# Kernel tuning notes

Hardware: AMD Instinct MI355X
Metric: run time of the kernel (lower is better)

## Reference

```python
import jax, jax.numpy as jnp
import numpy as np

N, M, E, DIM = 100000, 2000, 400000, 128
GIN = 2 * DIM + 3  # gate MLP input width


def _mlp2(x, W1, b1, W2, b2):
    # Linear -> ReLU -> Linear
    return jnp.maximum(x @ W1 + b1, 0.0) @ W2 + b2


def setup_inputs() -> dict:
    key = jax.random.key(0)
    ks = jax.random.split(key, 20)
    s = lambda fan_in: 1.0 / np.sqrt(fan_in)
    inp = {
        "res_feat": jax.random.normal(ks[0], (N, DIM), jnp.float32),
        "meta_feat": jax.random.normal(ks[1], (M, DIM), jnp.float32),
        "sec_ids": jax.random.randint(ks[2], (N,), 0, M),
        "batch_pe_vector": jax.random.normal(ks[3], (N, 3), jnp.float32),
        "batch_meta_2_node_edge": jax.random.randint(ks[4], (2, E), 0, M),
        "batch_meta_2_node_vector": jax.random.normal(ks[5], (E, 3), jnp.float32),
        # gate1 params
        "g1_W1": jax.random.uniform(ks[6], (GIN, DIM), jnp.float32, -s(GIN), s(GIN)),
        "g1_b1": jnp.zeros((DIM,), jnp.float32),
        "g1_W2": jax.random.uniform(ks[7], (DIM, DIM), jnp.float32, -s(DIM), s(DIM)),
        "g1_b2": jnp.zeros((DIM,), jnp.float32),
        # gate2 params
        "g2_W1": jax.random.uniform(ks[8], (GIN, DIM), jnp.float32, -s(GIN), s(GIN)),
        "g2_b1": jnp.zeros((DIM,), jnp.float32),
        "g2_W2": jax.random.uniform(ks[9], (DIM, DIM), jnp.float32, -s(DIM), s(DIM)),
        "g2_b2": jnp.zeros((DIM,), jnp.float32),
        # fuse params
        "f_W1": jax.random.uniform(ks[10], (DIM, DIM), jnp.float32, -s(DIM), s(DIM)),
        "f_b1": jnp.zeros((DIM,), jnp.float32),
        "f_W2": jax.random.uniform(ks[11], (DIM, DIM), jnp.float32, -s(DIM), s(DIM)),
        "f_b2": jnp.zeros((DIM,), jnp.float32),
    }
    return inp


def reference(res_feat, meta_feat, sec_ids, batch_pe_vector,
              batch_meta_2_node_edge, batch_meta_2_node_vector,
              g1_W1, g1_b1, g1_W2, g1_b2,
              g2_W1, g2_b1, g2_W2, g2_b2,
              f_W1, f_b1, f_W2, f_b2):
    n = res_feat.shape[0]
    # gate1: per-node gather of meta features
    meta_broadcast = meta_feat[sec_ids]                       # [N, dim]
    gate1_in = jnp.concatenate([res_feat, meta_broadcast, -batch_pe_vector], axis=-1)
    gate1_w = _mlp2(gate1_in, g1_W1, g1_b1, g1_W2, g1_b2)     # [N, dim]
    # gate2: per-edge gathers
    src, dst = batch_meta_2_node_edge[0], batch_meta_2_node_edge[1]
    meta_add = meta_feat[src]                                 # [E, dim]
    res_b = res_feat[dst]                                     # [E, dim]
    gate2_in = jnp.concatenate([res_b, meta_add, batch_meta_2_node_vector], axis=-1)
    gate2_w = _mlp2(gate2_in, g2_W1, g2_b1, g2_W2, g2_b2)     # [E, dim]
    # scatter_mean over destination nodes
    vals = gate2_w * meta_add
    sums = jax.ops.segment_sum(vals, dst, num_segments=n)
    cnts = jax.ops.segment_sum(jnp.ones((vals.shape[0],), vals.dtype), dst, num_segments=n)
    meta_add_fea = sums / jnp.maximum(cnts, 1.0)[:, None]
    fused = res_feat + gate1_w * meta_broadcast + meta_add_fea
    return _mlp2(fused, f_W1, f_b1, f_W2, f_b2)
```

## Files before the change

kernel.cpp:

```cpp
#include <hip/hip_runtime.h>


typedef short bf16x8 __attribute__((ext_vector_type(8)));
typedef float f32x4  __attribute__((ext_vector_type(4)));

#define XS_PAD 136

__device__ __forceinline__ unsigned short f2bf(float f){
  union { float f; unsigned u; } v; v.f = f;
  return (unsigned short)((v.u + 0x7FFFu + ((v.u >> 16) & 1u)) >> 16);
}
__device__ __forceinline__ unsigned pack2(float a, float b){
  return (unsigned)f2bf(a) | ((unsigned)f2bf(b) << 16);
}

__device__ __forceinline__ void mfma_layer(const unsigned short* Xs,
                                           const bf16x8 (&B)[2][4],
                                           int lane, f32x4 (&acc)[4][2]) {
  const int lcol = lane & 15, quad = lane >> 4;
  #pragma unroll
  for (int rg = 0; rg < 4; ++rg) {
    bf16x8 A[4];
    const unsigned short* ab = Xs + (rg*16 + lcol)*XS_PAD + quad*8;
    #pragma unroll
    for (int kk = 0; kk < 4; ++kk) A[kk] = *(const bf16x8*)(ab + kk*32);
    #pragma unroll
    for (int ctl = 0; ctl < 2; ++ctl)
      #pragma unroll
      for (int kk = 0; kk < 4; ++kk)
        acc[rg][ctl] = __builtin_amdgcn_mfma_f32_16x16x32_bf16(
            A[kk], B[ctl][kk], acc[rg][ctl], 0, 0, 0);
  }
}

__device__ __forceinline__ void load_bfrags(const unsigned short* __restrict__ Wt,
                                            int wave, int lane, bf16x8 (&B)[2][4]) {
  const int lcol = lane & 15, quad = lane >> 4;
  #pragma unroll
  for (int ctl = 0; ctl < 2; ++ctl) {
    int col = (wave*2 + ctl)*16 + lcol;
    #pragma unroll
    for (int kk = 0; kk < 4; ++kk)
      B[ctl][kk] = *(const bf16x8*)(Wt + (size_t)col*128 + kk*32 + quad*8);
  }
}

__device__ __forceinline__ void zero_acc(f32x4 (&acc)[4][2]) {
  #pragma unroll
  for (int rg = 0; rg < 4; ++rg)
    #pragma unroll
    for (int ctl = 0; ctl < 2; ++ctl) {
      acc[rg][ctl][0]=0.f; acc[rg][ctl][1]=0.f;
      acc[rg][ctl][2]=0.f; acc[rg][ctl][3]=0.f;
    }
}

struct WPtrs { const float* s[8]; };
__global__ __launch_bounds__(256) void transpose_w8(WPtrs p,
                                                    unsigned short* __restrict__ dstbase,
                                                    int* __restrict__ counts, int M) {
  int slab = blockIdx.x >> 4, blk = blockIdx.x & 15;
  const float* W = p.s[slab];
  unsigned short* Wt = dstbase + (size_t)slab*16384;
  int c  = blk*8 + (threadIdx.x >> 5);
  int k0 = (threadIdx.x & 31) * 4;
  unsigned short o[4];
  #pragma unroll
  for (int j = 0; j < 4; ++j) o[j] = f2bf(W[(size_t)(k0 + j)*128 + c]);
  *(uint2*)(Wt + (size_t)c*128 + k0) =
      make_uint2((unsigned)o[0] | ((unsigned)o[1] << 16),
                 (unsigned)o[2] | ((unsigned)o[3] << 16));
  int tid = blockIdx.x*256 + threadIdx.x;
  int tot = gridDim.x*256;
  for (int i = tid; i < M; i += tot) counts[i] = 0;
}

__global__ __launch_bounds__(256) void prep_and_hist(
    const float* __restrict__ res, const float* __restrict__ meta,
    const unsigned short* __restrict__ WAt, const unsigned short* __restrict__ WBt,
    const unsigned short* __restrict__ WCt, const float* __restrict__ b1,
    float* __restrict__ A2, float* __restrict__ M2, float* __restrict__ M1,
    int mrows, int nbPrep,
    const int* __restrict__ dst, int* __restrict__ counts, int E) {
  if ((int)blockIdx.x >= nbPrep) {
    int e = ((int)blockIdx.x - nbPrep)*256 + threadIdx.x;
    if (e < E) atomicAdd(&counts[dst[e]], 1);
    return;
  }
  __shared__ __align__(16) unsigned short Xs[64*XS_PAD];
  const int t = threadIdx.x, lane = t & 63, wave = t >> 6;
  const int quad = lane >> 4, lcol = lane & 15;
  const int third = nbPrep / 3;
  const int yy = (int)blockIdx.x / third;
  const int bx = (int)blockIdx.x - yy*third;
  const int tile0 = bx * 64;
  const float* X = (yy == 0) ? res : meta;
  const unsigned short* Wt = (yy == 0) ? WAt : (yy == 1) ? WBt : WCt;
  float* Y = (yy == 0) ? A2 : (yy == 1) ? M2 : M1;
  bf16x8 B[2][4];
  load_bfrags(Wt, wave, lane, B);
  #pragma unroll
  for (int i = 0; i < 8; ++i) {
    int f = t + i*256, row = f >> 5, c4 = f & 31;
    int gr = tile0 + row;
    float4 v = make_float4(0.f,0.f,0.f,0.f);
    if (gr < mrows) v = *(const float4*)(X + (size_t)gr*128 + c4*4);
    *(uint2*)(Xs + row*XS_PAD + c4*4) = make_uint2(pack2(v.x,v.y), pack2(v.z,v.w));
  }
  __syncthreads();
  f32x4 acc[4][2]; zero_acc(acc);
  mfma_layer(Xs, B, lane, acc);
  #pragma unroll
  for (int rg = 0; rg < 4; ++rg)
    #pragma unroll
    for (int ctl = 0; ctl < 2; ++ctl) {
      int col = (wave*2 + ctl)*16 + lcol;
      float badd = 0.f;
      if (yy == 0) badd = b1[col];
      #pragma unroll
      for (int reg = 0; reg < 4; ++reg) {
        int gr = tile0 + rg*16 + quad*4 + reg;
        if (gr < mrows) Y[(size_t)gr*128 + col] = acc[rg][ctl][reg] + badd;
      }
    }
}

__global__ __launch_bounds__(1024) void scan_all(const int* __restrict__ counts,
                                                 int* __restrict__ row_start,
                                                 int* __restrict__ cursor, int M) {
  __shared__ int s[1024];
  __shared__ int carry_s;
  const int t = threadIdx.x;
  if (t == 0) carry_s = 0;
  __syncthreads();
  for (int base = 0; base < M; base += 2048) {
    int i0 = base + 2*t, i1 = i0 + 1;
    int c0 = (i0 < M) ? counts[i0] : 0;
    int c1 = (i1 < M) ? counts[i1] : 0;
    int pair = c0 + c1;
    s[t] = pair; __syncthreads();
    for (int off = 1; off < 1024; off <<= 1) {
      int x = (t >= off) ? s[t-off] : 0; __syncthreads();
      s[t] += x; __syncthreads();
    }
    int carry = carry_s;
    int excl = carry + s[t] - pair;
    if (i0 < M) { row_start[i0] = excl;       cursor[i0] = excl; }
    if (i1 < M) { row_start[i1] = excl + c0;  cursor[i1] = excl + c0; }
    __syncthreads();
    if (t == 1023) carry_s = carry + s[1023];
    __syncthreads();
  }
}

__global__ void fill_kernel(const int* __restrict__ dst, const int* __restrict__ src,
                            const float* __restrict__ evec, int* __restrict__ cursor,
                            float4* __restrict__ edata, int E) {
  int e = blockIdx.x*256 + threadIdx.x;
  if (e < E) {
    int p = atomicAdd(&cursor[dst[e]], 1);
    edata[p] = make_float4(__int_as_float(src[e]),
                           evec[(size_t)e*3], evec[(size_t)e*3+1], evec[(size_t)e*3+2]);
  }
}

__global__ __launch_bounds__(256) void edge_mfma(
    const float* __restrict__ A2, const float* __restrict__ M2,
    const float* __restrict__ meta, const float4* __restrict__ edata,
    const int* __restrict__ row_start, const int* __restrict__ counts,
    const float* __restrict__ g2W1full,
    const unsigned short* __restrict__ W2t, const float* __restrict__ b2,
    float* __restrict__ SUM) {
  const int n = blockIdx.x;
  const int cnt = counts[n];
  if (cnt <= 0) return;
  const int rs = row_start[n];

  __shared__ __align__(16) unsigned short Xh[64*XS_PAD];
  __shared__ int srcl[64];
  __shared__ float evl[192];
  const int t = threadIdx.x, lane = t & 63, wave = t >> 6;
  const int quad = lane >> 4, lcol = lane & 15;
  const int c0 = (t & 31) * 4, rbase = t >> 5;

  float4 ed = make_float4(0.f,0.f,0.f,0.f);
  if (t < 64 && t < cnt) ed = edata[rs + t];

  bf16x8 BW2[2][4];
  load_bfrags(W2t, wave, lane, BW2);
  float4 base = *(const float4*)(A2 + (size_t)n*128 + c0);
  float4 w0 = *(const float4*)(g2W1full + 256*128 + c0);
  float4 w1 = *(const float4*)(g2W1full + 257*128 + c0);
  float4 w2 = *(const float4*)(g2W1full + 258*128 + c0);
  const int colA = wave*32 + lcol, colB = colA + 16;
  const float b2A = b2[colA], b2B = b2[colB];
  float psA = 0.f, psB = 0.f;

  for (int t0 = 0; t0 < cnt; t0 += 64) {
    if (t0) __syncthreads();
    if (t < 64) {
      srcl[t] = __float_as_int(ed.x);
      evl[3*t] = ed.y; evl[3*t+1] = ed.z; evl[3*t+2] = ed.w;
      int idx = t0 + 64 + t;
      ed = make_float4(0.f,0.f,0.f,0.f);
      if (idx < cnt) ed = edata[rs + idx];
    }
    __syncthreads();
    #pragma unroll
    for (int i = 0; i < 8; ++i) {
      int row = rbase + 8*i;
      float4 h = make_float4(0.f,0.f,0.f,0.f);
      if (t0 + row < cnt) {
        int s = srcl[row];
        float4 m = *(const float4*)(M2 + (size_t)s*128 + c0);
        float e0 = evl[3*row], e1 = evl[3*row+1], e2 = evl[3*row+2];
        h.x = fmaxf(base.x + m.x + e0*w0.x + e1*w1.x + e2*w2.x, 0.f);
        h.y = fmaxf(base.y + m.y + e0*w0.y + e1*w1.y + e2*w2.y, 0.f);
        h.z = fmaxf(base.z + m.z + e0*w0.z + e1*w1.z + e2*w2.z, 0.f);
        h.w = fmaxf(base.w + m.w + e0*w0.w + e1*w1.w + e2*w2.w, 0.f);
      }
      *(uint2*)(Xh + row*XS_PAD + c0) = make_uint2(pack2(h.x,h.y), pack2(h.z,h.w));
    }
    __syncthreads();
    f32x4 acc[4][2]; zero_acc(acc);
    mfma_layer(Xh, BW2, lane, acc);
    #pragma unroll
    for (int rg = 0; rg < 4; ++rg)
      #pragma unroll
      for (int reg = 0; reg < 4; ++reg) {
        int rl = rg*16 + quad*4 + reg;
        if (t0 + rl < cnt) {
          int s = srcl[rl];
          psA += (acc[rg][0][reg] + b2A) * meta[(size_t)s*128 + colA];
          psB += (acc[rg][1][reg] + b2B) * meta[(size_t)s*128 + colB];
        }
      }
  }
  psA += __shfl_xor(psA, 16, 64); psA += __shfl_xor(psA, 32, 64);
  psB += __shfl_xor(psB, 16, 64); psB += __shfl_xor(psB, 32, 64);
  if (quad == 0) {
    SUM[(size_t)n*128 + colA] = psA;
    SUM[(size_t)n*128 + colB] = psB;
  }
}

__global__ __launch_bounds__(256) void fused_node(
    const float* __restrict__ res, const float* __restrict__ meta,
    const int* __restrict__ sec_ids, const float* __restrict__ pe,
    const float* __restrict__ g1W1full, const float* __restrict__ M1,
    const unsigned short* __restrict__ g1At,
    const unsigned short* __restrict__ g1W2t, const float* __restrict__ g1b1,
    const float* __restrict__ g1b2,
    const unsigned short* __restrict__ fW1t, const float* __restrict__ fb1v,
    const unsigned short* __restrict__ fW2t, const float* __restrict__ fb2v,
    const float* __restrict__ SUM, const int* __restrict__ counts, int msize,
    float* __restrict__ out, int rows) {
  __shared__ __align__(16) unsigned short Xs[64*XS_PAD];
  __shared__ int   sids[64];
  __shared__ float pel[192];
  __shared__ float inv[64];
  const int t = threadIdx.x, lane = t & 63, wave = t >> 6;
  const int quad = lane >> 4, lcol = lane & 15;
  const int tile0 = blockIdx.x * 64;
  const int c0 = (t & 31) * 4, rbase = t >> 5;
  const int colA = wave*32 + lcol, colB = colA + 16;

  if (t < 64) {
    int gr = tile0 + t;
    sids[t] = (gr < rows) ? sec_ids[gr] : 0;
    float p0=0.f,p1=0.f,p2=0.f;
    if (gr < rows){ p0=pe[(size_t)gr*3]; p1=pe[(size_t)gr*3+1]; p2=pe[(size_t)gr*3+2]; }
    pel[3*t]=p0; pel[3*t+1]=p1; pel[3*t+2]=p2;
    int c = (gr < rows && gr < msize) ? counts[gr] : 0;
    inv[t] = (c > 0) ? 1.f/(float)c : 0.f;
  }
  bf16x8 BF[2][4];
  load_bfrags(g1At, wave, lane, BF);
  #pragma unroll
  for (int i = 0; i < 8; ++i) {
    int row = rbase + 8*i, gr = tile0 + row;
    float4 v = make_float4(0.f,0.f,0.f,0.f);
    if (gr < rows) v = *(const float4*)(res + (size_t)gr*128 + c0);
    *(uint2*)(Xs + row*XS_PAD + c0) = make_uint2(pack2(v.x,v.y), pack2(v.z,v.w));
  }
  __syncthreads();
  f32x4 acc[4][2]; zero_acc(acc);
  mfma_layer(Xs, BF, lane, acc);
  load_bfrags(g1W2t, wave, lane, BF);
  __syncthreads();
  {
    const float b1A = g1b1[colA], b1B = g1b1[colB];
    const float wA0 = g1W1full[256*128+colA], wA1 = g1W1full[257*128+colA],
                wA2 = g1W1full[258*128+colA];
    const float wB0 = g1W1full[256*128+colB], wB1 = g1W1full[257*128+colB],
                wB2 = g1W1full[258*128+colB];
    #pragma unroll
    for (int rg = 0; rg < 4; ++rg)
      #pragma unroll
      for (int reg = 0; reg < 4; ++reg) {
        int row = rg*16 + quad*4 + reg;
        int sid = sids[row];
        float m1A = M1[(size_t)sid*128 + colA];
        float m1B = M1[(size_t)sid*128 + colB];
        float p0 = pel[3*row], p1 = pel[3*row+1], p2 = pel[3*row+2];
        float vA = acc[rg][0][reg] + m1A + b1A - p0*wA0 - p1*wA1 - p2*wA2;
        float vB = acc[rg][1][reg] + m1B + b1B - p0*wB0 - p1*wB1 - p2*wB2;
        Xs[row*XS_PAD + colA] = f2bf(fmaxf(vA, 0.f));
        Xs[row*XS_PAD + colB] = f2bf(fmaxf(vB, 0.f));
      }
  }
  __syncthreads();
  zero_acc(acc);
  mfma_layer(Xs, BF, lane, acc);
  load_bfrags(fW1t, wave, lane, BF);
  __syncthreads();
  {
    const float b2A = g1b2[colA], b2B = g1b2[colB];
    #pragma unroll
    for (int rg = 0; rg < 4; ++rg)
      #pragma unroll
      for (int reg = 0; reg < 4; ++reg) {
        int row = rg*16 + quad*4 + reg, gr = tile0 + row;
        unsigned short oA = 0, oB = 0;
        if (gr < rows) {
          int sid = sids[row];
          float gA = acc[rg][0][reg] + b2A, gB = acc[rg][1][reg] + b2B;
          float mA = meta[(size_t)sid*128 + colA], mB = meta[(size_t)sid*128 + colB];
          float rA = res[(size_t)gr*128 + colA],  rB = res[(size_t)gr*128 + colB];
          float iv = inv[row];
          float sA = 0.f, sB = 0.f;
          if (iv > 0.f) {
            sA = SUM[(size_t)gr*128 + colA] * iv;
            sB = SUM[(size_t)gr*128 + colB] * iv;
          }
          oA = f2bf(rA + gA*mA + sA);
          oB = f2bf(rB + gB*mB + sB);
        }
        Xs[row*XS_PAD + colA] = oA;
        Xs[row*XS_PAD + colB] = oB;
      }
  }
  __syncthreads();
  zero_acc(acc);
  mfma_layer(Xs, BF, lane, acc);
  load_bfrags(fW2t, wave, lane, BF);
  __syncthreads();
  {
    const float fb1A = fb1v[colA], fb1B = fb1v[colB];
    #pragma unroll
    for (int rg = 0; rg < 4; ++rg)
      #pragma unroll
      for (int reg = 0; reg < 4; ++reg) {
        int row = rg*16 + quad*4 + reg;
        Xs[row*XS_PAD + colA] = f2bf(fmaxf(acc[rg][0][reg] + fb1A, 0.f));
        Xs[row*XS_PAD + colB] = f2bf(fmaxf(acc[rg][1][reg] + fb1B, 0.f));
      }
  }
  __syncthreads();
  zero_acc(acc);
  mfma_layer(Xs, BF, lane, acc);
  {
    const float fb2A = fb2v[colA], fb2B = fb2v[colB];
    #pragma unroll
    for (int rg = 0; rg < 4; ++rg)
      #pragma unroll
      for (int reg = 0; reg < 4; ++reg) {
        int gr = tile0 + rg*16 + quad*4 + reg;
        if (gr < rows) {
          out[(size_t)gr*128 + colA] = acc[rg][0][reg] + fb2A;
          out[(size_t)gr*128 + colB] = acc[rg][1][reg] + fb2B;
        }
      }
  }
}

extern "C" void kernel_launch(void* const* d_in, const int* in_sizes, int n_in,
                              void* d_out, int out_size, void* d_ws, size_t ws_size,
                              hipStream_t stream) {
  const float* res     = (const float*)d_in[0];
  const float* meta    = (const float*)d_in[1];
  const int*   sec_ids = (const int*)  d_in[2];
  const float* pe      = (const float*)d_in[3];
  const int*   edge    = (const int*)  d_in[4];
  const float* evec    = (const float*)d_in[5];
  const float* g1W1 = (const float*)d_in[6];
  const float* g1b1 = (const float*)d_in[7];
  const float* g1W2 = (const float*)d_in[8];
  const float* g1b2 = (const float*)d_in[9];
  const float* g2W1 = (const float*)d_in[10];
  const float* g2b1 = (const float*)d_in[11];
  const float* g2W2 = (const float*)d_in[12];
  const float* g2b2 = (const float*)d_in[13];
  const float* fW1  = (const float*)d_in[14];
  const float* fb1  = (const float*)d_in[15];
  const float* fW2  = (const float*)d_in[16];
  const float* fb2  = (const float*)d_in[17];

  const int N = in_sizes[0] / 128;
  const int M = in_sizes[1] / 128;
  const int E = in_sizes[4] / 2;
  const int* src = edge;
  const int* dst = edge + E;

  float* ws = (float*)d_ws;
  float* A2   = ws;
  float* M2   = A2 + (size_t)M*128;
  float* M1   = M2 + (size_t)M*128;
  float* SUMb = M1 + (size_t)M*128;
  int* counts     = (int*)(SUMb + (size_t)M*128);
  int* row_startp = counts + M;
  int* cursor     = row_startp + M;
  uintptr_t ap = (uintptr_t)(cursor + M);
  ap = (ap + 15) & ~(uintptr_t)15;
  float4* edata = (float4*)ap;
  uintptr_t wp = (uintptr_t)(edata + E);
  wp = (wp + 15) & ~(uintptr_t)15;
  unsigned short* Wt = (unsigned short*)wp;
  unsigned short* W_g1A  = Wt + 0*16384;
  unsigned short* W_g1B  = Wt + 1*16384;
  unsigned short* W_g1W2 = Wt + 2*16384;
  unsigned short* W_g2A  = Wt + 3*16384;
  unsigned short* W_g2B  = Wt + 4*16384;
  unsigned short* W_g2W2 = Wt + 5*16384;
  unsigned short* W_fW1  = Wt + 6*16384;
  unsigned short* W_fW2  = Wt + 7*16384;
  float* out = (float*)d_out;

  WPtrs p;
  p.s[0] = g1W1;            p.s[1] = g1W1 + 128*128;  p.s[2] = g1W2;
  p.s[3] = g2W1;            p.s[4] = g2W1 + 128*128;  p.s[5] = g2W2;
  p.s[6] = fW1;             p.s[7] = fW2;

  const int nbMt   = (M + 63) / 64;
  const int nbN    = (N + 63) / 64;
  const int nbE    = (E + 255) / 256;
  const int nbPrep = 3*nbMt;

  transpose_w8<<<128, 256, 0, stream>>>(p, Wt, counts, M);
  prep_and_hist<<<nbPrep + nbE, 256, 0, stream>>>(res, meta, W_g2A, W_g2B, W_g1B,
                                                  g2b1, A2, M2, M1, M, nbPrep,
                                                  dst, counts, E);
  scan_all<<<1, 1024, 0, stream>>>(counts, row_startp, cursor, M);
  fill_kernel<<<nbE, 256, 0, stream>>>(dst, src, evec, cursor, edata, E);
  edge_mfma<<<M, 256, 0, stream>>>(A2, M2, meta, edata, row_startp, counts,
                                   g2W1, W_g2W2, g2b2, SUMb);
  fused_node<<<nbN, 256, 0, stream>>>(res, meta, sec_ids, pe, g1W1, M1,
                                      W_g1A, W_g1W2, g1b1, g1b2,
                                      W_fW1, fb1, W_fW2, fb2,
                                      SUMb, counts, M, out, N);
}
```

Baseline: 375.3 us.

## Fold scan into histogram via last-block ticket; prefetch gathers and double-buffer LDS

```diff
diff --git a/kernel.cpp b/kernel.cpp
--- a/kernel.cpp
+++ b/kernel.cpp
@@ -58,7 +58,8 @@
 struct WPtrs { const float* s[8]; };
 __global__ __launch_bounds__(256) void transpose_w8(WPtrs p,
                                                     unsigned short* __restrict__ dstbase,
-                                                    int* __restrict__ counts, int M) {
+                                                    int* __restrict__ counts,
+                                                    int* __restrict__ ticket, int M) {
   int slab = blockIdx.x >> 4, blk = blockIdx.x & 15;
   const float* W = p.s[slab];
   unsigned short* Wt = dstbase + (size_t)slab*16384;
@@ -73,22 +74,53 @@
   int tid = blockIdx.x*256 + threadIdx.x;
   int tot = gridDim.x*256;
   for (int i = tid; i < M; i += tot) counts[i] = 0;
-}
-
-__global__ __launch_bounds__(256) void prep_and_hist(
+  if (tid == 0) *ticket = 0;
+}
+
+__global__ __launch_bounds__(256) void prep_hist_scan(
     const float* __restrict__ res, const float* __restrict__ meta,
     const unsigned short* __restrict__ WAt, const unsigned short* __restrict__ WBt,
     const unsigned short* __restrict__ WCt, const float* __restrict__ b1,
     float* __restrict__ A2, float* __restrict__ M2, float* __restrict__ M1,
     int mrows, int nbPrep,
-    const int* __restrict__ dst, int* __restrict__ counts, int E) {
+    const int* __restrict__ dst, int* __restrict__ counts, int E,
+    int* __restrict__ ticket, int nbHist,
+    int* __restrict__ row_start, int* __restrict__ cursor, int M) {
+  const int t = threadIdx.x;
   if ((int)blockIdx.x >= nbPrep) {
-    int e = ((int)blockIdx.x - nbPrep)*256 + threadIdx.x;
+    int e = ((int)blockIdx.x - nbPrep)*256 + t;
     if (e < E) atomicAdd(&counts[dst[e]], 1);
+    __threadfence();
+    __syncthreads();
+    __shared__ int lastFlag;
+    if (t == 0) {
+      int old = __hip_atomic_fetch_add(ticket, 1, __ATOMIC_ACQ_REL,
+                                       __HIP_MEMORY_SCOPE_AGENT);
+      lastFlag = (old == nbHist - 1);
+    }
+    __syncthreads();
+    if (!lastFlag) return;
+    __shared__ int ssum[256];
+    int carry = 0;
+    for (int base = 0; base < M; base += 256) {
+      int i = base + t;
+      int v = 0;
+      if (i < M) v = __hip_atomic_load(&counts[i], __ATOMIC_RELAXED,
+                                       __HIP_MEMORY_SCOPE_AGENT);
+      ssum[t] = v; __syncthreads();
+      for (int off = 1; off < 256; off <<= 1) {
+        int x = (t >= off) ? ssum[t-off] : 0; __syncthreads();
+        ssum[t] += x; __syncthreads();
+      }
+      int excl = carry + ssum[t] - v;
+      if (i < M) { row_start[i] = excl; cursor[i] = excl; }
+      carry += ssum[255];
+      __syncthreads();
+    }
     return;
   }
   __shared__ __align__(16) unsigned short Xs[64*XS_PAD];
-  const int t = threadIdx.x, lane = t & 63, wave = t >> 6;
+  const int lane = t & 63, wave = t >> 6;
   const int quad = lane >> 4, lcol = lane & 15;
   const int third = nbPrep / 3;
   const int yy = (int)blockIdx.x / third;
@@ -123,34 +155,6 @@
         if (gr < mrows) Y[(size_t)gr*128 + col] = acc[rg][ctl][reg] + badd;
       }
     }
-}
-
-__global__ __launch_bounds__(1024) void scan_all(const int* __restrict__ counts,
-                                                 int* __restrict__ row_start,
-                                                 int* __restrict__ cursor, int M) {
-  __shared__ int s[1024];
-  __shared__ int carry_s;
-  const int t = threadIdx.x;
-  if (t == 0) carry_s = 0;
-  __syncthreads();
-  for (int base = 0; base < M; base += 2048) {
-    int i0 = base + 2*t, i1 = i0 + 1;
-    int c0 = (i0 < M) ? counts[i0] : 0;
-    int c1 = (i1 < M) ? counts[i1] : 0;
-    int pair = c0 + c1;
-    s[t] = pair; __syncthreads();
-    for (int off = 1; off < 1024; off <<= 1) {
-      int x = (t >= off) ? s[t-off] : 0; __syncthreads();
-      s[t] += x; __syncthreads();
-    }
-    int carry = carry_s;
-    int excl = carry + s[t] - pair;
-    if (i0 < M) { row_start[i0] = excl;       cursor[i0] = excl; }
-    if (i1 < M) { row_start[i1] = excl + c0;  cursor[i1] = excl + c0; }
-    __syncthreads();
-    if (t == 1023) carry_s = carry + s[1023];
-    __syncthreads();
-  }
 }
 
 __global__ void fill_kernel(const int* __restrict__ dst, const int* __restrict__ src,
@@ -206,6 +210,16 @@
       if (idx < cnt) ed = edata[rs + idx];
     }
     __syncthreads();
+    float mvA[16], mvB[16];
+    #pragma unroll
+    for (int rg = 0; rg < 4; ++rg)
+      #pragma unroll
+      for (int reg = 0; reg < 4; ++reg) {
+        int k = rg*4 + reg, rl = rg*16 + quad*4 + reg;
+        int s = srcl[rl];
+        mvA[k] = meta[(size_t)s*128 + colA];
+        mvB[k] = meta[(size_t)s*128 + colB];
+      }
     #pragma unroll
     for (int i = 0; i < 8; ++i) {
       int row = rbase + 8*i;
@@ -228,11 +242,10 @@
     for (int rg = 0; rg < 4; ++rg)
       #pragma unroll
       for (int reg = 0; reg < 4; ++reg) {
-        int rl = rg*16 + quad*4 + reg;
+        int k = rg*4 + reg, rl = rg*16 + quad*4 + reg;
         if (t0 + rl < cnt) {
-          int s = srcl[rl];
-          psA += (acc[rg][0][reg] + b2A) * meta[(size_t)s*128 + colA];
-          psB += (acc[rg][1][reg] + b2B) * meta[(size_t)s*128 + colB];
+          psA += (acc[rg][0][reg] + b2A) * mvA[k];
+          psB += (acc[rg][1][reg] + b2B) * mvB[k];
         }
       }
   }
@@ -255,7 +268,8 @@
     const unsigned short* __restrict__ fW2t, const float* __restrict__ fb2v,
     const float* __restrict__ SUM, const int* __restrict__ counts, int msize,
     float* __restrict__ out, int rows) {
-  __shared__ __align__(16) unsigned short Xs[64*XS_PAD];
+  __shared__ __align__(16) unsigned short Xa[64*XS_PAD];
+  __shared__ __align__(16) unsigned short Xb[64*XS_PAD];
   __shared__ int   sids[64];
   __shared__ float pel[192];
   __shared__ float inv[64];
@@ -281,13 +295,23 @@
     int row = rbase + 8*i, gr = tile0 + row;
     float4 v = make_float4(0.f,0.f,0.f,0.f);
     if (gr < rows) v = *(const float4*)(res + (size_t)gr*128 + c0);
-    *(uint2*)(Xs + row*XS_PAD + c0) = make_uint2(pack2(v.x,v.y), pack2(v.z,v.w));
+    *(uint2*)(Xa + row*XS_PAD + c0) = make_uint2(pack2(v.x,v.y), pack2(v.z,v.w));
   }
   __syncthreads();
+
+  float m1A[16], m1B[16];
+  #pragma unroll
+  for (int rg = 0; rg < 4; ++rg)
+    #pragma unroll
+    for (int reg = 0; reg < 4; ++reg) {
+      int k = rg*4 + reg, row = rg*16 + quad*4 + reg;
+      int sid = sids[row];
+      m1A[k] = M1[(size_t)sid*128 + colA];
+      m1B[k] = M1[(size_t)sid*128 + colB];
+    }
   f32x4 acc[4][2]; zero_acc(acc);
-  mfma_layer(Xs, BF, lane, acc);
+  mfma_layer(Xa, BF, lane, acc);
   load_bfrags(g1W2t, wave, lane, BF);
-  __syncthreads();
   {
     const float b1A = g1b1[colA], b1B = g1b1[colB];
     const float wA0 = g1W1full[256*128+colA], wA1 = g1W1full[257*128+colA],
@@ -298,53 +322,54 @@
     for (int rg = 0; rg < 4; ++rg)
       #pragma unroll
       for (int reg = 0; reg < 4; ++reg) {
-        int row = rg*16 + quad*4 + reg;
-        int sid = sids[row];
-        float m1A = M1[(size_t)sid*128 + colA];
-        float m1B = M1[(size_t)sid*128 + colB];
+        int k = rg*4 + reg, row = rg*16 + quad*4 + reg;
         float p0 = pel[3*row], p1 = pel[3*row+1], p2 = pel[3*row+2];
-        float vA = acc[rg][0][reg] + m1A + b1A - p0*wA0 - p1*wA1 - p2*wA2;
-        float vB = acc[rg][1][reg] + m1B + b1B - p0*wB0 - p1*wB1 - p2*wB2;
-        Xs[row*XS_PAD + colA] = f2bf(fmaxf(vA, 0.f));
-        Xs[row*XS_PAD + colB] = f2bf(fmaxf(vB, 0.f));
+        float vA = acc[rg][0][reg] + m1A[k] + b1A - p0*wA0 - p1*wA1 - p2*wA2;
+        float vB = acc[rg][1][reg] + m1B[k] + b1B - p0*wB0 - p1*wB1 - p2*wB2;
+        Xb[row*XS_PAD + colA] = f2bf(fmaxf(vA, 0.f));
+        Xb[row*XS_PAD + colB] = f2bf(fmaxf(vB, 0.f));
       }
   }
   __syncthreads();
+
+  float sAv[16], sBv[16];
+  #pragma unroll
+  for (int rg = 0; rg < 4; ++rg)
+    #pragma unroll
+    for (int reg = 0; reg < 4; ++reg) {
+      int k = rg*4 + reg, row = rg*16 + quad*4 + reg, gr = tile0 + row;
+      float iv = inv[row];
+      sAv[k] = (iv > 0.f) ? SUM[(size_t)gr*128 + colA] : 0.f;
+      sBv[k] = (iv > 0.f) ? SUM[(size_t)gr*128 + colB] : 0.f;
+    }
   zero_acc(acc);
-  mfma_layer(Xs, BF, lane, acc);
+  mfma_layer(Xb, BF, lane, acc);
   load_bfrags(fW1t, wave, lane, BF);
-  __syncthreads();
   {
     const float b2A = g1b2[colA], b2B = g1b2[colB];
     #pragma unroll
     for (int rg = 0; rg < 4; ++rg)
       #pragma unroll
       for (int reg = 0; reg < 4; ++reg) {
-        int row = rg*16 + quad*4 + reg, gr = tile0 + row;
+        int k = rg*4 + reg, row = rg*16 + quad*4 + reg, gr = tile0 + row;
         unsigned short oA = 0, oB = 0;
         if (gr < rows) {
           int sid = sids[row];
+          float iv = inv[row];
           float gA = acc[rg][0][reg] + b2A, gB = acc[rg][1][reg] + b2B;
           float mA = meta[(size_t)sid*128 + colA], mB = meta[(size_t)sid*128 + colB];
           float rA = res[(size_t)gr*128 + colA],  rB = res[(size_t)gr*128 + colB];
-          float iv = inv[row];
-          float sA = 0.f, sB = 0.f;
-          if (iv > 0.f) {
-            sA = SUM[(size_t)gr*128 + colA] * iv;
-            sB = SUM[(size_t)gr*128 + colB] * iv;
-          }
-          oA = f2bf(rA + gA*mA + sA);
-          oB = f2bf(rB + gB*mB + sB);
+          oA = f2bf(rA + gA*mA + sAv[k]*iv);
+          oB = f2bf(rB + gB*mB + sBv[k]*iv);
         }
-        Xs[row*XS_PAD + colA] = oA;
-        Xs[row*XS_PAD + colB] = oB;
+        Xa[row*XS_PAD + colA] = oA;
+        Xa[row*XS_PAD + colB] = oB;
       }
   }
   __syncthreads();
   zero_acc(acc);
-  mfma_layer(Xs, BF, lane, acc);
+  mfma_layer(Xa, BF, lane, acc);
   load_bfrags(fW2t, wave, lane, BF);
-  __syncthreads();
   {
     const float fb1A = fb1v[colA], fb1B = fb1v[colB];
     #pragma unroll
@@ -352,13 +377,13 @@
       #pragma unroll
       for (int reg = 0; reg < 4; ++reg) {
         int row = rg*16 + quad*4 + reg;
-        Xs[row*XS_PAD + colA] = f2bf(fmaxf(acc[rg][0][reg] + fb1A, 0.f));
-        Xs[row*XS_PAD + colB] = f2bf(fmaxf(acc[rg][1][reg] + fb1B, 0.f));
+        Xb[row*XS_PAD + colA] = f2bf(fmaxf(acc[rg][0][reg] + fb1A, 0.f));
+        Xb[row*XS_PAD + colB] = f2bf(fmaxf(acc[rg][1][reg] + fb1B, 0.f));
       }
   }
   __syncthreads();
   zero_acc(acc);
-  mfma_layer(Xs, BF, lane, acc);
+  mfma_layer(Xb, BF, lane, acc);
   {
     const float fb2A = fb2v[colA], fb2B = fb2v[colB];
     #pragma unroll
@@ -410,7 +435,8 @@
   int* counts     = (int*)(SUMb + (size_t)M*128);
   int* row_startp = counts + M;
   int* cursor     = row_startp + M;
-  uintptr_t ap = (uintptr_t)(cursor + M);
+  int* ticket     = cursor + M;
+  uintptr_t ap = (uintptr_t)(ticket + 4);
   ap = (ap + 15) & ~(uintptr_t)15;
   float4* edata = (float4*)ap;
   uintptr_t wp = (uintptr_t)(edata + E);
@@ -436,11 +462,12 @@
   const int nbE    = (E + 255) / 256;
   const int nbPrep = 3*nbMt;
 
-  transpose_w8<<<128, 256, 0, stream>>>(p, Wt, counts, M);
-  prep_and_hist<<<nbPrep + nbE, 256, 0, stream>>>(res, meta, W_g2A, W_g2B, W_g1B,
-                                                  g2b1, A2, M2, M1, M, nbPrep,
-                                                  dst, counts, E);
-  scan_all<<<1, 1024, 0, stream>>>(counts, row_startp, cursor, M);
+  transpose_w8<<<128, 256, 0, stream>>>(p, Wt, counts, ticket, M);
+  prep_hist_scan<<<nbPrep + nbE, 256, 0, stream>>>(res, meta, W_g2A, W_g2B, W_g1B,
+                                                   g2b1, A2, M2, M1, M, nbPrep,
+                                                   dst, counts, E,
+                                                   ticket, nbE,
+                                                   row_startp, cursor, M);
   fill_kernel<<<nbE, 256, 0, stream>>>(dst, src, evec, cursor, edata, E);
   edge_mfma<<<M, 256, 0, stream>>>(A2, M2, meta, edata, row_startp, counts,
                                    g2W1, W_g2W2, g2b2, SUMb);
```

After: 461.0 us. 22.8% more time.
